# Optimization experiments

Measured on AMD Instinct MI355X. Metric: run time of the kernel, lower is better.

The kernel has to match this reference:

```python
import jax, jax.numpy as jnp
import numpy as np

MAX_ITER = 10
EPS = 0.01


def setup_inputs() -> dict:
    key = jax.random.key(0)
    ks = jax.random.split(key, 6)
    B, D, H, O = 4096, 512, 1024, 512
    return {
        "x": jax.random.normal(ks[0], (B, D), jnp.float32),
        "prev_hidden": jax.random.normal(ks[1], (B, H), jnp.float32) * 0.1,
        "prev_ponder": jnp.zeros((B, 1), jnp.float32),
        "prev_steps": jnp.zeros((B, 1), jnp.float32),
        "W_ih": jax.random.normal(ks[2], (H, D + 1), jnp.float32) * 0.02,
        "b_ih": jnp.zeros((H,), jnp.float32),
        "W_hh": jax.random.normal(ks[3], (H, H), jnp.float32) * 0.02,
        "b_hh": jnp.zeros((H,), jnp.float32),
        "W_halt": jax.random.normal(ks[4], (1, H), jnp.float32) * 0.1,
        "b_halt": jnp.zeros((1,), jnp.float32),
        "W_ans": jax.random.normal(ks[5], (O, H), jnp.float32) * 0.02,
        "b_ans": jnp.zeros((O,), jnp.float32),
    }


def reference(x, prev_hidden, prev_ponder, prev_steps,
              W_ih, b_ih, W_hh, b_hh, W_halt, b_halt, W_ans, b_ans):
    B = x.shape[0]
    O = W_ans.shape[0]

    def controller(x_n, s):  # vanilla tanh RNN cell (cfg.MODEL.LSTM=False)
        return jnp.tanh(x_n @ W_ih.T + b_ih + s @ W_hh.T + b_hh)

    def halting_step(carry, inp):
        flag, n = inp  # n is the 1-based loop index (float), flag=1 only at n==1
        s_n, s_acc, y, h, r_n, R, N, steps = carry
        x_n = jnp.concatenate([x, jnp.full((B, 1), flag, x.dtype)], axis=1)
        s_new = controller(x_n, s_n)                       # [B, H]
        h_n = jax.nn.sigmoid(s_new @ W_halt.T + b_halt)    # [B, 1]
        y_n = s_new @ W_ans.T + b_ans                      # [B, O]
        h = h + h_n
        isN = h >= (1.0 - EPS)                             # halted mask (frozen once true)
        p_n = jnp.where(isN, r_n, h_n)                     # remainder at halting step, else h_n
        y = y + p_n * y_n
        s_acc = s_acc + p_n * s_new
        steps = jnp.where(isN, steps, steps + 1.0)
        r_new = jnp.where(isN, jnp.zeros((), x.dtype), 1.0 - h)
        R_new = jnp.where(isN, R, r_new)
        N_new = jnp.where(isN, N, n + 1.0)
        return (s_new, s_acc, y, h, r_new, R_new, N_new, steps), None

    carry0 = (
        prev_hidden,                          # s_n
        jnp.zeros_like(prev_hidden),          # s accumulator
        jnp.zeros((B, O), x.dtype),           # y
        jnp.zeros((B, 1), x.dtype),           # h (halt prob mass)
        jnp.ones((B, 1), x.dtype),            # r_n
        jnp.ones((B, 1), x.dtype),            # R
        jnp.zeros((B, 1), x.dtype),           # N
        prev_steps + 1.0,                     # steps
    )
    ns = jnp.arange(1, MAX_ITER, dtype=x.dtype)
    flags = (ns == 1).astype(x.dtype)
    carry, _ = jax.lax.scan(halting_step, carry0, (flags, ns))
    s_n, s_acc, y, h, r_n, R, N, steps = carry

    # final (remainder) step, flag = 1 only if MAX_ITER == 1
    final_flag = 1.0 if MAX_ITER == 1 else 0.0
    x_n = jnp.concatenate([x, jnp.full((B, 1), final_flag, x.dtype)], axis=1)
    s_new = controller(x_n, s_n)
    y_n = s_new @ W_ans.T + b_ans
    p_n = r_n                                 # remainder (0 for already-halted rows)
    y = y + p_n * y_n
    s_acc = s_acc + p_n * s_new
    ponder_cost = prev_ponder + R + N
    return (y, s_acc, ponder_cost, steps)
```

## Files before the change

kernel.cpp:

```cpp
#include <hip/hip_runtime.h>
#include <cmath>
#include <cstddef>


#define MAX_ITER 10

typedef short bf16x8 __attribute__((ext_vector_type(8)));
typedef float f32x4  __attribute__((ext_vector_type(4)));

__device__ __forceinline__ ushort f2bf(float f) {
    unsigned u = __float_as_uint(f);
    u += 0x7fff + ((u >> 16) & 1);
    return (ushort)(u >> 16);
}
__device__ __forceinline__ float bf2f(ushort b) {
    return __uint_as_float(((unsigned)b) << 16);
}
__device__ __forceinline__ void gld16(const void* g, void* l) {
    __builtin_amdgcn_global_load_lds(
        (const __attribute__((address_space(1))) void*)g,
        (__attribute__((address_space(3))) void*)l, 16, 0, 0);
}

template<int BM, int BN, int MODE>
__device__ __forceinline__ void gemm_body(
    int bx, int by,
    const ushort* __restrict__ ahi, const ushort* __restrict__ alo, int lda,
    const ushort* __restrict__ bhi, const ushort* __restrict__ blo, int ldb,
    int tps, float* __restrict__ Cout, int ldn,
    const float* __restrict__ e0, const float* __restrict__ e1, float flag,
    const ushort* __restrict__ uA, const ushort* __restrict__ uB,
    ushort* __restrict__ shiO, ushort* __restrict__ sloO,
    ushort* smem)
{
    constexpr int FRM = BM / 32;
    constexpr int FRN = BN / 32;
    constexpr int NL  = (BM + BN) / 32;
    ushort* As = smem;
    ushort* Bs = smem + 3 * BM * 64;

    const int tid  = threadIdx.x;
    const int lane = tid & 63;
    const int wave = tid >> 6;
    const int lq   = lane & 15;
    const int kh   = lane >> 4;
    const int wr0  = (wave >> 1) * (BM / 2);
    const int wc0  = (wave & 1) * (BN / 2);
    const int m0   = bx * BM;
    const int n0   = by * BN;

    f32x4 acc[FRM][FRN];
#pragma unroll
    for (int r = 0; r < FRM; ++r)
#pragma unroll
        for (int c = 0; c < FRN; ++c) acc[r][c] = (f32x4)0.f;

    const int steps = 3 * tps;

    auto stage = [&](int buf, int t) {
        const int seg = (t >= 2 * tps) ? 2 : ((t >= tps) ? 1 : 0);
        const int k0  = (t - seg * tps) * 64;
        const ushort* aS = (seg == 2) ? alo : ahi;
        const ushort* bS = (seg == 1) ? blo : bhi;
#pragma unroll
        for (int j = 0; j < BM / 32; ++j) {
            int c   = j * 256 + tid;
            int row = c >> 3;
            int kb  = ((c & 7) << 4) ^ ((row & 7) << 4);
            gld16(aS + (size_t)(m0 + row) * lda + k0 + (kb >> 1),
                  As + buf * (BM * 64) + (size_t)(j * 256 + (tid & ~63)) * 8);
        }
#pragma unroll
        for (int j = 0; j < BN / 32; ++j) {
            int c   = j * 256 + tid;
            int row = c >> 3;
            int kb  = ((c & 7) << 4) ^ ((row & 7) << 4);
            gld16(bS + (size_t)(n0 + row) * ldb + k0 + (kb >> 1),
                  Bs + buf * (BN * 64) + (size_t)(j * 256 + (tid & ~63)) * 8);
        }
    };

    stage(0, 0);
    stage(1, 1);
    stage(2, 2);

    int cur = 0;
    for (int t = 0; t < steps; ++t) {
        const int rem = steps - 1 - t;
        if (rem >= 2)      __builtin_amdgcn_s_waitcnt(0xF70 | (2 * NL));
        else if (rem == 1) __builtin_amdgcn_s_waitcnt(0xF70 | NL);
        else               __builtin_amdgcn_s_waitcnt(0xF70);
        __builtin_amdgcn_sched_barrier(0);
        __builtin_amdgcn_s_barrier();
        __builtin_amdgcn_sched_barrier(0);

        const ushort* Ab = As + cur * (BM * 64);
        const ushort* Bb = Bs + cur * (BN * 64);
#pragma unroll
        for (int kt = 0; kt < 2; ++kt) {
            bf16x8 af[FRM], bfr[FRN];
#pragma unroll
            for (int r = 0; r < FRM; ++r) {
                int row = wr0 + r * 16 + lq;
                int kb  = (kt * 64 + kh * 16) ^ ((row & 7) << 4);
                af[r] = *reinterpret_cast<const bf16x8*>(&Ab[row * 64 + (kb >> 1)]);
            }
#pragma unroll
            for (int c = 0; c < FRN; ++c) {
                int row = wc0 + c * 16 + lq;
                int kb  = (kt * 64 + kh * 16) ^ ((row & 7) << 4);
                bfr[c] = *reinterpret_cast<const bf16x8*>(&Bb[row * 64 + (kb >> 1)]);
            }
            __builtin_amdgcn_s_setprio(1);
#pragma unroll
            for (int r = 0; r < FRM; ++r)
#pragma unroll
                for (int c = 0; c < FRN; ++c)
                    acc[r][c] = __builtin_amdgcn_mfma_f32_16x16x32_bf16(
                        af[r], bfr[c], acc[r][c], 0, 0, 0);
            __builtin_amdgcn_s_setprio(0);
        }
        __builtin_amdgcn_sched_barrier(0);
        __builtin_amdgcn_s_barrier();
        __builtin_amdgcn_sched_barrier(0);
        if (t + 3 < steps) stage(cur, t + 3);
        cur = (cur == 2) ? 0 : cur + 1;
    }

#pragma unroll
    for (int r = 0; r < FRM; ++r)
#pragma unroll
        for (int c = 0; c < FRN; ++c) {
            const size_t col = n0 + wc0 + c * 16 + lq;
#pragma unroll
            for (int q = 0; q < 4; ++q) {
                const size_t row = m0 + wr0 + r * 16 + kh * 4 + q;
                float v = acc[r][c][q];
                if constexpr (MODE == 0) {
                    v += e0[col] + e1[col];
                    ushort hb = f2bf(v);
                    ushort lb = f2bf(v - bf2f(hb));
                    shiO[row * ldn + col] = hb;
                    sloO[row * ldn + col] = lb;
                } else if constexpr (MODE == 1) {
                    v += bf2f(uA[row * ldn + col]) + bf2f(uB[row * ldn + col]);
                    if (flag != 0.f) v += flag * e1[col];
                    float s = tanhf(v);
                    ushort hb = f2bf(s);
                    ushort lb = f2bf(s - bf2f(hb));
                    shiO[row * ldn + col] = hb;
                    sloO[row * ldn + col] = lb;
                } else {
                    Cout[row * ldn + col] = v + e1[row] * e0[col];
                }
            }
        }
}

template<int BM, int BN, int MODE>
__global__ __launch_bounds__(256)
void mfma_gemm(int gx,
               const ushort* __restrict__ ahi, const ushort* __restrict__ alo, int lda,
               const ushort* __restrict__ bhi, const ushort* __restrict__ blo, int ldb,
               int tps, float* __restrict__ Cout, int ldn,
               const float* __restrict__ e0, const float* __restrict__ e1,
               float flag,
               const ushort* __restrict__ uA, const ushort* __restrict__ uB,
               ushort* __restrict__ shiO, ushort* __restrict__ sloO)
{
    __shared__ __align__(16) ushort smem[3 * (BM + BN) * 64];
    const int n = gridDim.x;
    const int b = blockIdx.x;
    const int w = (b & 7) * (n >> 3) + (b >> 3);
    gemm_body<BM, BN, MODE>(w % gx, w / gx, ahi, alo, lda, bhi, blo, ldb,
                            tps, Cout, ldn, e0, e1, flag, uA, uB,
                            shiO, sloO, smem);
}

__global__ void init_kernel(float* __restrict__ sacc_zero, size_t nzero,
                            float* __restrict__ hA, float* __restrict__ rA,
                            float* __restrict__ RA, float* __restrict__ NA,
                            float* __restrict__ stA, float* __restrict__ pAcc,
                            const float* __restrict__ prev_steps, int B)
{
    size_t i = (size_t)blockIdx.x * 256 + threadIdx.x;
    if (i < nzero) sacc_zero[i] = 0.f;
    if (i < (size_t)B) {
        hA[i] = 0.f; rA[i] = 1.f; RA[i] = 1.f; NA[i] = 0.f;
        stA[i] = prev_steps[i] + 1.f; pAcc[i] = 0.f;
    }
}

__global__ void split_f32(const float* __restrict__ src,
                          ushort* __restrict__ hi, ushort* __restrict__ lo, size_t n4)
{
    size_t i = (size_t)blockIdx.x * 256 + threadIdx.x;
    if (i < n4) {
        float4 v = reinterpret_cast<const float4*>(src)[i];
        ushort4 h, l;
        h.x = f2bf(v.x); l.x = f2bf(v.x - bf2f(h.x));
        h.y = f2bf(v.y); l.y = f2bf(v.y - bf2f(h.y));
        h.z = f2bf(v.z); l.z = f2bf(v.z - bf2f(h.z));
        h.w = f2bf(v.w); l.w = f2bf(v.w - bf2f(h.w));
        reinterpret_cast<ushort4*>(hi)[i] = h;
        reinterpret_cast<ushort4*>(lo)[i] = l;
    }
}

__global__ void wih_split(const float* __restrict__ Wih,
                          ushort* __restrict__ hi, ushort* __restrict__ lo,
                          float* __restrict__ wcol, int H, int D)
{
    size_t i = (size_t)blockIdx.x * 256 + threadIdx.x;
    if (i < (size_t)H * D) {
        int h = (int)(i / D), d = (int)(i % D);
        float v = Wih[(size_t)h * (D + 1) + d];
        ushort hb = f2bf(v);
        hi[i] = hb; lo[i] = f2bf(v - bf2f(hb));
    }
    if (i < (size_t)H) wcol[i] = Wih[i * (size_t)(D + 1) + D];
}

__global__ __launch_bounds__(256)
void halt_update(const ushort* __restrict__ shi, const ushort* __restrict__ slo,
                 const float* __restrict__ Whalt, const float* __restrict__ bhalt,
                 float* __restrict__ hA, float* __restrict__ rA, float* __restrict__ RA,
                 float* __restrict__ NA, float* __restrict__ stA,
                 float* __restrict__ pAcc,
                 float* __restrict__ s_acc,
                 ushort* __restrict__ fsHi, ushort* __restrict__ fsLo,
                 float n1, int H, int isFinal)
{
    const int b = blockIdx.x;
    const int tid = threadIdx.x;
    const size_t base = (size_t)b * H;
    const int i = tid * 4;
    ushort4 h4 = *reinterpret_cast<const ushort4*>(shi + base + i);
    ushort4 l4 = *reinterpret_cast<const ushort4*>(slo + base + i);
    float s0 = bf2f(h4.x) + bf2f(l4.x);
    float s1 = bf2f(h4.y) + bf2f(l4.y);
    float s2 = bf2f(h4.z) + bf2f(l4.z);
    float s3 = bf2f(h4.w) + bf2f(l4.w);

    __shared__ float partial[4];
    __shared__ float psh;
    float4 w4 = *reinterpret_cast<const float4*>(Whalt + i);
    float lsum = s0 * w4.x + s1 * w4.y + s2 * w4.z + s3 * w4.w;
#pragma unroll
    for (int off = 32; off > 0; off >>= 1) lsum += __shfl_down(lsum, off, 64);
    if ((tid & 63) == 0) partial[tid >> 6] = lsum;
    __syncthreads();
    if (tid == 0) {
        float pv;
        if (isFinal) {
            pv = rA[b];
        } else {
            float dot = partial[0] + partial[1] + partial[2] + partial[3] + bhalt[0];
            float h_n = 1.f / (1.f + expf(-dot));
            float hh = hA[b] + h_n;
            bool isN = hh >= 0.99f;
            pv = isN ? rA[b] : h_n;
            float r_new = isN ? 0.f : 1.f - hh;
            if (!isN) { RA[b] = r_new; NA[b] = n1; stA[b] += 1.f; }
            hA[b] = hh; rA[b] = r_new;
        }
        pAcc[b] += pv;
        psh = pv;
    }
    __syncthreads();
    const float pv = psh;
    float4* sac = reinterpret_cast<float4*>(s_acc + base + i);
    if (!isFinal) {
        if (pv != 0.f) {
            float4 o = *sac;
            o.x = fmaf(pv, s0, o.x); o.y = fmaf(pv, s1, o.y);
            o.z = fmaf(pv, s2, o.z); o.w = fmaf(pv, s3, o.w);
            *sac = o;
        }
    } else {
        float4 o = *sac;
        o.x = fmaf(pv, s0, o.x); o.y = fmaf(pv, s1, o.y);
        o.z = fmaf(pv, s2, o.z); o.w = fmaf(pv, s3, o.w);
        *sac = o;
        ushort4 fh, fl;
        fh.x = f2bf(o.x); fl.x = f2bf(o.x - bf2f(fh.x));
        fh.y = f2bf(o.y); fl.y = f2bf(o.y - bf2f(fh.y));
        fh.z = f2bf(o.z); fl.z = f2bf(o.z - bf2f(fh.z));
        fh.w = f2bf(o.w); fl.w = f2bf(o.w - bf2f(fh.w));
        *reinterpret_cast<ushort4*>(fsHi + base + i) = fh;
        *reinterpret_cast<ushort4*>(fsLo + base + i) = fl;
    }
}

__global__ void finalize_kernel(const float* __restrict__ pp, const float* __restrict__ RA,
                                const float* __restrict__ NA, const float* __restrict__ stA,
                                float* __restrict__ pon, float* __restrict__ stp, int B)
{
    int i = blockIdx.x * 256 + threadIdx.x;
    if (i < B) { pon[i] = pp[i] + RA[i] + NA[i]; stp[i] = stA[i]; }
}

extern "C" void kernel_launch(void* const* d_in, const int* in_sizes, int n_in,
                              void* d_out, int out_size, void* d_ws, size_t ws_size,
                              hipStream_t stream)
{
    const float* x     = (const float*)d_in[0];
    const float* ph    = (const float*)d_in[1];
    const float* pp    = (const float*)d_in[2];
    const float* ps    = (const float*)d_in[3];
    const float* Wih   = (const float*)d_in[4];
    const float* bih   = (const float*)d_in[5];
    const float* Whh   = (const float*)d_in[6];
    const float* bhh   = (const float*)d_in[7];
    const float* Whalt = (const float*)d_in[8];
    const float* bhalt = (const float*)d_in[9];
    const float* Wans  = (const float*)d_in[10];
    const float* bans  = (const float*)d_in[11];

    const int B = in_sizes[2];
    const int H = in_sizes[5];
    const int O = in_sizes[11];
    const int D = in_sizes[0] / B;

    float* out_y   = (float*)d_out;
    float* out_sac = out_y + (size_t)B * O;
    float* out_pon = out_sac + (size_t)B * H;
    float* out_stp = out_pon + B;

    char* w = (char*)d_ws;
    ushort* xpHi = (ushort*)w; w += (size_t)B * H * 2;
    ushort* xpLo = (ushort*)w; w += (size_t)B * H * 2;
    ushort* shi[2], *slo[2];
    shi[0] = (ushort*)w; w += (size_t)B * H * 2;
    slo[0] = (ushort*)w; w += (size_t)B * H * 2;
    shi[1] = (ushort*)w; w += (size_t)B * H * 2;
    slo[1] = (ushort*)w; w += (size_t)B * H * 2;
    ushort* whhhi = (ushort*)w; w += (size_t)H * H * 2;
    ushort* whhlo = (ushort*)w; w += (size_t)H * H * 2;
    ushort* wanshi = (ushort*)w; w += (size_t)O * H * 2;
    ushort* wanslo = (ushort*)w; w += (size_t)O * H * 2;
    ushort* wihhi = (ushort*)w; w += (size_t)H * D * 2;
    ushort* wihlo = (ushort*)w; w += (size_t)H * D * 2;
    float* wcol = (float*)w; w += (size_t)H * 4;
    float* hA   = (float*)w; w += (size_t)B * 4;
    float* rA   = (float*)w; w += (size_t)B * 4;
    float* RA   = (float*)w; w += (size_t)B * 4;
    float* NA   = (float*)w; w += (size_t)B * 4;
    float* stA  = (float*)w; w += (size_t)B * 4;
    float* pAcc = (float*)w; w += (size_t)B * 4;

    ushort* xhi = shi[1];
    ushort* xlo = slo[1];
    ushort* sacHi = xpHi;
    ushort* sacLo = xpLo;

    init_kernel<<<(unsigned)(((size_t)B * H + 255) / 256), 256, 0, stream>>>(
        out_sac, (size_t)B * H, hA, rA, RA, NA, stA, pAcc, ps, B);

    split_f32<<<(unsigned)(((size_t)B * D / 4 + 255) / 256), 256, 0, stream>>>(x, xhi, xlo, (size_t)B * D / 4);
    split_f32<<<(unsigned)(((size_t)B * H / 4 + 255) / 256), 256, 0, stream>>>(ph, shi[0], slo[0], (size_t)B * H / 4);
    split_f32<<<(unsigned)(((size_t)H * H / 4 + 255) / 256), 256, 0, stream>>>(Whh, whhhi, whhlo, (size_t)H * H / 4);
    split_f32<<<(unsigned)(((size_t)O * H / 4 + 255) / 256), 256, 0, stream>>>(Wans, wanshi, wanslo, (size_t)O * H / 4);
    wih_split<<<(unsigned)(((size_t)H * D + 255) / 256), 256, 0, stream>>>(Wih, wihhi, wihlo, wcol, H, D);

    mfma_gemm<64, 128, 0><<<(B / 64) * (H / 128), 256, 0, stream>>>(
        B / 64, xhi, xlo, D, wihhi, wihlo, D, D / 64,
        nullptr, H, bih, bhh, 0.f, nullptr, nullptr, xpHi, xpLo);

    mfma_gemm<64, 128, 1><<<(B / 64) * (H / 128), 256, 0, stream>>>(
        B / 64, shi[0], slo[0], H, whhhi, whhlo, H, H / 64,
        nullptr, H, nullptr, wcol, 1.f, xpHi, xpLo, shi[1], slo[1]);

    int cur = 1;
    for (int t = 1; t < MAX_ITER; t++) {
        halt_update<<<B, 256, 0, stream>>>(
            shi[cur], slo[cur], Whalt, bhalt, hA, rA, RA, NA, stA, pAcc,
            out_sac, nullptr, nullptr, (float)(t + 1), H, 0);
        mfma_gemm<64, 128, 1><<<(B / 64) * (H / 128), 256, 0, stream>>>(
            B / 64, shi[cur], slo[cur], H, whhhi, whhlo, H, H / 64,
            nullptr, H, nullptr, wcol, 0.f, xpHi, xpLo, shi[cur ^ 1], slo[cur ^ 1]);
        cur ^= 1;
    }

    halt_update<<<B, 256, 0, stream>>>(
        shi[cur], slo[cur], Whalt, bhalt, hA, rA, RA, NA, stA, pAcc,
        out_sac, sacHi, sacLo, 0.f, H, 1);

    mfma_gemm<64, 64, 3><<<(B / 64) * (O / 64), 256, 0, stream>>>(
        B / 64, sacHi, sacLo, H, wanshi, wanslo, H, H / 64,
        out_y, O, bans, pAcc, 0.f, nullptr, nullptr, nullptr, nullptr);

    finalize_kernel<<<(B + 255) / 256, 256, 0, stream>>>(
        pp, RA, NA, stA, out_pon, out_stp, B);
}
```

Baseline: 713.6 us.

## Merge halting update into recurrent GEMM launch and store input projection in fp32

Each loop iteration now launches a single kernel whose first blocks do the halting dot product and s_acc accumulation (64 rows per block, 4 threads per row) while the remaining blocks do the W_hh GEMM on the same hidden state. The goal is to let the halt work overlap the GEMM and to remove one launch per step. The input projection is kept as a single fp32 buffer instead of hi/lo bf16 pairs, which simplifies the GEMM epilogue at the same memory footprint. The XCD block mapping is reworked into a helper. The merged kernel sizes shared memory dynamically, and the halt blocks get the same LDS allocation they never use, which may reduce occupancy.

```diff
diff --git a/kernel.cpp b/kernel.cpp
--- a/kernel.cpp
+++ b/kernel.cpp
@@ -20,6 +20,13 @@
     __builtin_amdgcn_global_load_lds(
         (const __attribute__((address_space(1))) void*)g,
         (__attribute__((address_space(3))) void*)l, 16, 0, 0);
+}
+
+__device__ __forceinline__ void xcd_map(int b, int gx, int& bx, int& by) {
+    const int c = gx >> 3;
+    const int l = b >> 3;
+    bx = (b & 7) * c + (l % c);
+    by = l / c;
 }
 
 template<int BM, int BN, int MODE>
@@ -29,7 +36,6 @@
     const ushort* __restrict__ bhi, const ushort* __restrict__ blo, int ldb,
     int tps, float* __restrict__ Cout, int ldn,
     const float* __restrict__ e0, const float* __restrict__ e1, float flag,
-    const ushort* __restrict__ uA, const ushort* __restrict__ uB,
     ushort* __restrict__ shiO, ushort* __restrict__ sloO,
     ushort* smem)
 {
@@ -137,13 +143,9 @@
                 const size_t row = m0 + wr0 + r * 16 + kh * 4 + q;
                 float v = acc[r][c][q];
                 if constexpr (MODE == 0) {
-                    v += e0[col] + e1[col];
-                    ushort hb = f2bf(v);
-                    ushort lb = f2bf(v - bf2f(hb));
-                    shiO[row * ldn + col] = hb;
-                    sloO[row * ldn + col] = lb;
+                    Cout[row * ldn + col] = v + e0[col] + e1[col];
                 } else if constexpr (MODE == 1) {
-                    v += bf2f(uA[row * ldn + col]) + bf2f(uB[row * ldn + col]);
+                    v += e0[row * ldn + col];
                     if (flag != 0.f) v += flag * e1[col];
                     float s = tanhf(v);
                     ushort hb = f2bf(s);
@@ -164,17 +166,85 @@
                const ushort* __restrict__ bhi, const ushort* __restrict__ blo, int ldb,
                int tps, float* __restrict__ Cout, int ldn,
                const float* __restrict__ e0, const float* __restrict__ e1,
-               float flag,
-               const ushort* __restrict__ uA, const ushort* __restrict__ uB,
-               ushort* __restrict__ shiO, ushort* __restrict__ sloO)
+               float flag, ushort* __restrict__ shiO, ushort* __restrict__ sloO)
 {
     __shared__ __align__(16) ushort smem[3 * (BM + BN) * 64];
-    const int n = gridDim.x;
+    int bx, by;
+    xcd_map(blockIdx.x, gx, bx, by);
+    gemm_body<BM, BN, MODE>(bx, by, ahi, alo, lda, bhi, blo, ldb,
+                            tps, Cout, ldn, e0, e1, flag, shiO, sloO, smem);
+}
+
+__device__ __forceinline__ void halt_rows(
+    int blk,
+    const ushort* __restrict__ shi, const ushort* __restrict__ slo,
+    const float* __restrict__ Whalt, const float* __restrict__ bhalt,
+    float* __restrict__ hA, float* __restrict__ rA, float* __restrict__ RA,
+    float* __restrict__ NA, float* __restrict__ stA, float* __restrict__ pAcc,
+    float* __restrict__ s_acc, float n1, int H)
+{
+    const int tid = threadIdx.x;
+    const int row = blk * 64 + (tid >> 2);
+    const int c0  = (tid & 3) * (H / 4);
+    const size_t base = (size_t)row * H + c0;
+
+    float dot = 0.f;
+    for (int i = 0; i < H / 4; i += 4) {
+        ushort4 h4 = *reinterpret_cast<const ushort4*>(shi + base + i);
+        ushort4 l4 = *reinterpret_cast<const ushort4*>(slo + base + i);
+        float4  w4 = *reinterpret_cast<const float4*>(Whalt + c0 + i);
+        dot += (bf2f(h4.x) + bf2f(l4.x)) * w4.x + (bf2f(h4.y) + bf2f(l4.y)) * w4.y
+             + (bf2f(h4.z) + bf2f(l4.z)) * w4.z + (bf2f(h4.w) + bf2f(l4.w)) * w4.w;
+    }
+    dot += __shfl_xor(dot, 1, 64);
+    dot += __shfl_xor(dot, 2, 64);
+
+    float h_n = 1.f / (1.f + expf(-(dot + bhalt[0])));
+    float hh  = hA[row] + h_n;
+    bool  isN = hh >= 0.99f;
+    float pv  = isN ? rA[row] : h_n;
+    float r_new = isN ? 0.f : 1.f - hh;
+    if ((tid & 3) == 0) {
+        if (!isN) { RA[row] = r_new; NA[row] = n1; stA[row] += 1.f; }
+        hA[row] = hh; rA[row] = r_new; pAcc[row] += pv;
+    }
+    if (pv != 0.f) {
+        for (int i = 0; i < H / 4; i += 4) {
+            ushort4 h4 = *reinterpret_cast<const ushort4*>(shi + base + i);
+            ushort4 l4 = *reinterpret_cast<const ushort4*>(slo + base + i);
+            float4 o = *reinterpret_cast<float4*>(s_acc + base + i);
+            o.x = fmaf(pv, bf2f(h4.x) + bf2f(l4.x), o.x);
+            o.y = fmaf(pv, bf2f(h4.y) + bf2f(l4.y), o.y);
+            o.z = fmaf(pv, bf2f(h4.z) + bf2f(l4.z), o.z);
+            o.w = fmaf(pv, bf2f(h4.w) + bf2f(l4.w), o.w);
+            *reinterpret_cast<float4*>(s_acc + base + i) = o;
+        }
+    }
+}
+
+__global__ __launch_bounds__(256)
+void merged_step(int hblks, int gx,
+                 const ushort* __restrict__ s_hi, const ushort* __restrict__ s_lo,
+                 const ushort* __restrict__ whhhi, const ushort* __restrict__ whhlo,
+                 int H, int tps,
+                 const float* __restrict__ xproj, const float* __restrict__ wcol,
+                 ushort* __restrict__ o_hi, ushort* __restrict__ o_lo,
+                 const float* __restrict__ Whalt, const float* __restrict__ bhalt,
+                 float* __restrict__ hA, float* __restrict__ rA, float* __restrict__ RA,
+                 float* __restrict__ NA, float* __restrict__ stA,
+                 float* __restrict__ pAcc, float* __restrict__ s_acc, float n1)
+{
+    extern __shared__ ushort smem[];
     const int b = blockIdx.x;
-    const int w = (b & 7) * (n >> 3) + (b >> 3);
-    gemm_body<BM, BN, MODE>(w % gx, w / gx, ahi, alo, lda, bhi, blo, ldb,
-                            tps, Cout, ldn, e0, e1, flag, uA, uB,
-                            shiO, sloO, smem);
+    if (b < hblks) {
+        halt_rows(b, s_hi, s_lo, Whalt, bhalt, hA, rA, RA, NA, stA, pAcc,
+                  s_acc, n1, H);
+    } else {
+        int bx, by;
+        xcd_map(b - hblks, gx, bx, by);
+        gemm_body<64, 128, 1>(bx, by, s_hi, s_lo, H, whhhi, whhlo, H, tps,
+                              nullptr, H, xproj, wcol, 0.f, o_hi, o_lo, smem);
+    }
 }
 
 __global__ void init_kernel(float* __restrict__ sacc_zero, size_t nzero,
@@ -222,74 +292,32 @@
 }
 
 __global__ __launch_bounds__(256)
-void halt_update(const ushort* __restrict__ shi, const ushort* __restrict__ slo,
-                 const float* __restrict__ Whalt, const float* __restrict__ bhalt,
-                 float* __restrict__ hA, float* __restrict__ rA, float* __restrict__ RA,
-                 float* __restrict__ NA, float* __restrict__ stA,
-                 float* __restrict__ pAcc,
-                 float* __restrict__ s_acc,
-                 ushort* __restrict__ fsHi, ushort* __restrict__ fsLo,
-                 float n1, int H, int isFinal)
+void final_halt(const ushort* __restrict__ shi, const ushort* __restrict__ slo,
+                const float* __restrict__ rA, float* __restrict__ pAcc,
+                float* __restrict__ s_acc,
+                ushort* __restrict__ fsHi, ushort* __restrict__ fsLo, int H)
 {
     const int b = blockIdx.x;
     const int tid = threadIdx.x;
     const size_t base = (size_t)b * H;
     const int i = tid * 4;
+    const float pv = rA[b];
+    if (tid == 0) pAcc[b] += pv;
     ushort4 h4 = *reinterpret_cast<const ushort4*>(shi + base + i);
     ushort4 l4 = *reinterpret_cast<const ushort4*>(slo + base + i);
-    float s0 = bf2f(h4.x) + bf2f(l4.x);
-    float s1 = bf2f(h4.y) + bf2f(l4.y);
-    float s2 = bf2f(h4.z) + bf2f(l4.z);
-    float s3 = bf2f(h4.w) + bf2f(l4.w);
-
-    __shared__ float partial[4];
-    __shared__ float psh;
-    float4 w4 = *reinterpret_cast<const float4*>(Whalt + i);
-    float lsum = s0 * w4.x + s1 * w4.y + s2 * w4.z + s3 * w4.w;
-#pragma unroll
-    for (int off = 32; off > 0; off >>= 1) lsum += __shfl_down(lsum, off, 64);
-    if ((tid & 63) == 0) partial[tid >> 6] = lsum;
-    __syncthreads();
-    if (tid == 0) {
-        float pv;
-        if (isFinal) {
-            pv = rA[b];
-        } else {
-            float dot = partial[0] + partial[1] + partial[2] + partial[3] + bhalt[0];
-            float h_n = 1.f / (1.f + expf(-dot));
-            float hh = hA[b] + h_n;
-            bool isN = hh >= 0.99f;
-            pv = isN ? rA[b] : h_n;
-            float r_new = isN ? 0.f : 1.f - hh;
-            if (!isN) { RA[b] = r_new; NA[b] = n1; stA[b] += 1.f; }
-            hA[b] = hh; rA[b] = r_new;
-        }
-        pAcc[b] += pv;
-        psh = pv;
-    }
-    __syncthreads();
-    const float pv = psh;
-    float4* sac = reinterpret_cast<float4*>(s_acc + base + i);
-    if (!isFinal) {
-        if (pv != 0.f) {
-            float4 o = *sac;
-            o.x = fmaf(pv, s0, o.x); o.y = fmaf(pv, s1, o.y);
-            o.z = fmaf(pv, s2, o.z); o.w = fmaf(pv, s3, o.w);
-            *sac = o;
-        }
-    } else {
-        float4 o = *sac;
-        o.x = fmaf(pv, s0, o.x); o.y = fmaf(pv, s1, o.y);
-        o.z = fmaf(pv, s2, o.z); o.w = fmaf(pv, s3, o.w);
-        *sac = o;
-        ushort4 fh, fl;
-        fh.x = f2bf(o.x); fl.x = f2bf(o.x - bf2f(fh.x));
-        fh.y = f2bf(o.y); fl.y = f2bf(o.y - bf2f(fh.y));
-        fh.z = f2bf(o.z); fl.z = f2bf(o.z - bf2f(fh.z));
-        fh.w = f2bf(o.w); fl.w = f2bf(o.w - bf2f(fh.w));
-        *reinterpret_cast<ushort4*>(fsHi + base + i) = fh;
-        *reinterpret_cast<ushort4*>(fsLo + base + i) = fl;
-    }
+    float4 o = *reinterpret_cast<const float4*>(s_acc + base + i);
+    o.x = fmaf(pv, bf2f(h4.x) + bf2f(l4.x), o.x);
+    o.y = fmaf(pv, bf2f(h4.y) + bf2f(l4.y), o.y);
+    o.z = fmaf(pv, bf2f(h4.z) + bf2f(l4.z), o.z);
+    o.w = fmaf(pv, bf2f(h4.w) + bf2f(l4.w), o.w);
+    *reinterpret_cast<float4*>(s_acc + base + i) = o;
+    ushort4 fh, fl;
+    fh.x = f2bf(o.x); fl.x = f2bf(o.x - bf2f(fh.x));
+    fh.y = f2bf(o.y); fl.y = f2bf(o.y - bf2f(fh.y));
+    fh.z = f2bf(o.z); fl.z = f2bf(o.z - bf2f(fh.z));
+    fh.w = f2bf(o.w); fl.w = f2bf(o.w - bf2f(fh.w));
+    *reinterpret_cast<ushort4*>(fsHi + base + i) = fh;
+    *reinterpret_cast<ushort4*>(fsLo + base + i) = fl;
 }
 
 __global__ void finalize_kernel(const float* __restrict__ pp, const float* __restrict__ RA,
@@ -328,8 +356,7 @@
     float* out_stp = out_pon + B;
 
     char* w = (char*)d_ws;
-    ushort* xpHi = (ushort*)w; w += (size_t)B * H * 2;
-    ushort* xpLo = (ushort*)w; w += (size_t)B * H * 2;
+    float* xproj = (float*)w;  w += (size_t)B * H * 4;
     ushort* shi[2], *slo[2];
     shi[0] = (ushort*)w; w += (size_t)B * H * 2;
     slo[0] = (ushort*)w; w += (size_t)B * H * 2;
@@ -351,8 +378,8 @@
 
     ushort* xhi = shi[1];
     ushort* xlo = slo[1];
-    ushort* sacHi = xpHi;
-    ushort* sacLo = xpLo;
+    ushort* sacHi = (ushort*)xproj;
+    ushort* sacLo = sacHi + (size_t)B * H;
 
     init_kernel<<<(unsigned)(((size_t)B * H + 255) / 256), 256, 0, stream>>>(
         out_sac, (size_t)B * H, hA, rA, RA, NA, stA, pAcc, ps, B);
@@ -365,30 +392,31 @@
 
     mfma_gemm<64, 128, 0><<<(B / 64) * (H / 128), 256, 0, stream>>>(
         B / 64, xhi, xlo, D, wihhi, wihlo, D, D / 64,
-        nullptr, H, bih, bhh, 0.f, nullptr, nullptr, xpHi, xpLo);
+        xproj, H, bih, bhh, 0.f, nullptr, nullptr);
 
     mfma_gemm<64, 128, 1><<<(B / 64) * (H / 128), 256, 0, stream>>>(
         B / 64, shi[0], slo[0], H, whhhi, whhlo, H, H / 64,
-        nullptr, H, nullptr, wcol, 1.f, xpHi, xpLo, shi[1], slo[1]);
+        nullptr, H, xproj, wcol, 1.f, shi[1], slo[1]);
+
+    const int hblks = B / 64;
+    const int gblks = (B / 64) * (H / 128);
+    const size_t lds_m = 3u * (64 + 128) * 64 * sizeof(ushort);
 
     int cur = 1;
     for (int t = 1; t < MAX_ITER; t++) {
-        halt_update<<<B, 256, 0, stream>>>(
-            shi[cur], slo[cur], Whalt, bhalt, hA, rA, RA, NA, stA, pAcc,
-            out_sac, nullptr, nullptr, (float)(t + 1), H, 0);
-        mfma_gemm<64, 128, 1><<<(B / 64) * (H / 128), 256, 0, stream>>>(
-            B / 64, shi[cur], slo[cur], H, whhhi, whhlo, H, H / 64,
-            nullptr, H, nullptr, wcol, 0.f, xpHi, xpLo, shi[cur ^ 1], slo[cur ^ 1]);
+        merged_step<<<hblks + gblks, 256, lds_m, stream>>>(
+            hblks, B / 64, shi[cur], slo[cur], whhhi, whhlo, H, H / 64,
+            xproj, wcol, shi[cur ^ 1], slo[cur ^ 1],
+            Whalt, bhalt, hA, rA, RA, NA, stA, pAcc, out_sac, (float)(t + 1));
         cur ^= 1;
     }
 
-    halt_update<<<B, 256, 0, stream>>>(
-        shi[cur], slo[cur], Whalt, bhalt, hA, rA, RA, NA, stA, pAcc,
-        out_sac, sacHi, sacLo, 0.f, H, 1);
+    final_halt<<<B, 256, 0, stream>>>(
+        shi[cur], slo[cur], rA, pAcc, out_sac, sacHi, sacLo, H);
 
     mfma_gemm<64, 64, 3><<<(B / 64) * (O / 64), 256, 0, stream>>>(
         B / 64, sacHi, sacLo, H, wanshi, wanslo, H, H / 64,
-        out_y, O, bans, pAcc, 0.f, nullptr, nullptr, nullptr, nullptr);
+        out_y, O, bans, pAcc, 0.f, nullptr, nullptr);
 
     finalize_kernel<<<(B + 255) / 256, 256, 0, stream>>>(
         pp, RA, NA, stA, out_pon, out_stp, B);
```

New measurement: 969.8 us. 35.9% more time.
